# Performance work log

Hardware: AMD Instinct MI355X
Metric: run time of the kernel (lower is better)

The kernel has to match this reference:

```python
import jax, jax.numpy as jnp
import numpy as np

N = 20000      # atoms
E = 320000     # directed edges
F = 128        # feat_dim
NRBF = 20
CUTOFF = 5.0
L = 3          # num_conv
EPS = 1e-15


def swish(x):
    return x * jax.nn.sigmoid(x)


def rbf(dist):
    # PainnRadialBasis: sin(n*pi*d/cutoff)/d, n = 1..NRBF
    n = jnp.arange(1, NRBF + 1, dtype=dist.dtype)
    d = dist[:, None]
    return jnp.sin(n * (jnp.pi / CUTOFF) * d) / d


def cos_envelope(dist):
    return jnp.where(dist < CUTOFF, 0.5 * (jnp.cos(jnp.pi * dist / CUTOFF) + 1.0), 0.0)


def vnorm(v):
    # NFF norm: sqrt(sum(v**2 + EPS))
    return jnp.sqrt(jnp.sum(v * v + EPS, axis=-1))


def setup_inputs() -> dict:
    key = jax.random.key(0)
    ks = jax.random.split(key, 32)
    s = 0.05
    inp = {
        'xyz': jax.random.uniform(ks[0], (N, 3), dtype=jnp.float32),
        'z': jax.random.randint(ks[1], (N,), 0, 100),
        'nbrs': jax.random.randint(ks[2], (E, 2), 0, N),
        # embedding + top-level DistEmb (n_rbf -> F)
        'embed_table': jax.random.normal(ks[3], (100, F), jnp.float32) * s,
        'de_w': jax.random.normal(ks[4], (NRBF, F), jnp.float32) * s,
        'de_b': jax.random.normal(ks[5], (F,), jnp.float32) * s,
        # message blocks (stacked over L layers)
        'msg_w1': jax.random.normal(ks[6], (L, F, F), jnp.float32) * s,
        'msg_b1': jax.random.normal(ks[7], (L, F), jnp.float32) * s,
        'msg_w2': jax.random.normal(ks[8], (L, F, 3 * F), jnp.float32) * s,
        'msg_b2': jax.random.normal(ks[9], (L, 3 * F), jnp.float32) * s,
        'msg_dw': jax.random.normal(ks[10], (L, NRBF, 3 * F), jnp.float32) * s,
        'msg_db': jax.random.normal(ks[11], (L, 3 * F), jnp.float32) * s,
        # update blocks
        'upd_u': jax.random.normal(ks[12], (L, F, F), jnp.float32) * s,
        'upd_v': jax.random.normal(ks[13], (L, F, F), jnp.float32) * s,
        'upd_w1': jax.random.normal(ks[14], (L, 2 * F, F), jnp.float32) * s,
        'upd_b1': jax.random.normal(ks[15], (L, F), jnp.float32) * s,
        'upd_w2': jax.random.normal(ks[16], (L, F, 3 * F), jnp.float32) * s,
        'upd_b2': jax.random.normal(ks[17], (L, 3 * F), jnp.float32) * s,
        # edge update MLPs
        'edge_w1': jax.random.normal(ks[18], (L, F, 2 * F), jnp.float32) * s,
        'edge_b1': jax.random.normal(ks[19], (L, 2 * F), jnp.float32) * s,
        'edge_w2': jax.random.normal(ks[20], (L, 2 * F, F), jnp.float32) * s,
        'edge_b2': jax.random.normal(ks[21], (L, F), jnp.float32) * s,
        # edge readout
        'ro_w1': jax.random.normal(ks[22], (F, 2 * F), jnp.float32) * s,
        'ro_b1': jax.random.normal(ks[23], (2 * F,), jnp.float32) * s,
        'ro_w2': jax.random.normal(ks[24], (2 * F, 1), jnp.float32) * s,
        'ro_b2': jax.random.normal(ks[25], (1,), jnp.float32) * s,
    }
    return inp


def forcepai_forward(xyz, embed_table, de_w, de_b, msg_w1, msg_b1, msg_w2, msg_b2,
                     msg_dw, msg_db, upd_u, upd_v, upd_w1, upd_b1, upd_w2, upd_b2,
                     edge_w1, edge_b1, edge_w2, edge_b2, ro_w1, ro_b1, ro_w2, ro_b2,
                     z, nbrs):
    seg = lambda x, idx: jax.ops.segment_sum(x, idx, num_segments=N)
    src, dst = nbrs[:, 0], nbrs[:, 1]

    r_ij = xyz[dst] - xyz[src]                       # (E, 3)
    dist = vnorm(r_ij)                               # (E,)
    unit = r_ij / dist[:, None]                      # (E, 3) == xyz_adjoint

    rbf_feats = rbf(dist)                            # (E, NRBF)
    env = cos_envelope(dist)[:, None]                # (E, 1)

    s_i = embed_table[z]                             # (N, F)
    v_i = jnp.zeros((N, F, 3), dtype=s_i.dtype)      # (N, F, 3)
    e_ij = (rbf_feats @ de_w + de_b) * env           # (E, F)

    for l in range(L):
        # --- MessageBlock ---
        phi = swish(s_i @ msg_w1[l] + msg_b1[l]) @ msg_w2[l] + msg_b2[l]   # (N, 3F)
        w_s = (rbf_feats @ msg_dw[l] + msg_db[l]) * env                    # (E, 3F)
        inv = (phi[dst] * w_s).reshape(E, 3, F)                            # (E, 3, F)
        split0 = inv[:, 0, :][..., None]                                   # (E, F, 1)
        split1 = inv[:, 1, :]                                              # (E, F)
        split2 = inv[:, 2, :][..., None]                                   # (E, F, 1)
        dv_ij = split2 * unit[:, None, :] + split0 * v_i[dst]              # (E, F, 3)
        s_i = s_i + seg(split1, src)
        v_i = v_i + seg(dv_ij, src)

        # --- UpdateBlock ---
        u_v = jnp.einsum('nfd,fg->ngd', v_i, upd_u[l])                     # (N, F, 3)
        v_v = jnp.einsum('nfd,fg->ngd', v_i, upd_v[l])                     # (N, F, 3)
        stack = jnp.concatenate([s_i, vnorm(v_v)], axis=-1)                # (N, 2F)
        split = (swish(stack @ upd_w1[l] + upd_b1[l]) @ upd_w2[l] + upd_b2[l]).reshape(N, 3, F)
        a_vv = split[:, 0, :][..., None]
        a_sv = split[:, 1, :]
        a_ss = split[:, 2, :]
        v_i = v_i + u_v * a_vv
        s_i = s_i + jnp.sum(u_v * v_v, axis=-1) * a_sv + a_ss

        # --- edge update ---
        pair = s_i[src] + s_i[dst]                                         # (E, F)
        e_ij = e_ij + (swish(pair @ edge_w1[l] + edge_b1[l]) @ edge_w2[l] + edge_b2[l])

    f_edge = (swish(e_ij @ ro_w1 + ro_b1) @ ro_w2 + ro_b2) * unit          # (E, 3)
    f_atom = seg(f_edge, src) - seg(f_edge, dst)                           # (N, 3)
    return f_atom


def reference(xyz, z, nbrs, embed_table, de_w, de_b, msg_w1, msg_b1, msg_w2, msg_b2,
              msg_dw, msg_db, upd_u, upd_v, upd_w1, upd_b1, upd_w2, upd_b2,
              edge_w1, edge_b1, edge_w2, edge_b2, ro_w1, ro_b1, ro_w2, ro_b2):
    return forcepai_forward(xyz, embed_table, de_w, de_b, msg_w1, msg_b1, msg_w2, msg_b2,
                            msg_dw, msg_db, upd_u, upd_v, upd_w1, upd_b1, upd_w2, upd_b2,
                            edge_w1, edge_b1, edge_w2, edge_b2, ro_w1, ro_b1, ro_w2, ro_b2,
                            z, nbrs)
```

## Files before the change

kernel.cpp:

```cpp
#include <hip/hip_runtime.h>

#define NA 20000
#define NE 320000
#define FD 128
#define NRBF 20
#define NL 3
#define PI_F 3.14159265358979323846f

typedef __attribute__((ext_vector_type(8))) short bf16x8;
typedef __attribute__((ext_vector_type(4))) float f32x4;

__device__ float g_unitv[NE*3];
__device__ float g_env[NE];
__device__ float g_rbf[NE*NRBF];
__device__ float g_eij[NE*FD];
__device__ float g_s[NA*FD];
__device__ float g_vA[NA*3*FD];
__device__ float g_vB[NA*3*FD];
__device__ float g_phi[NA*3*FD];
__device__ float g_vv[NA*3*FD];
__device__ float g_stk[NA*2*FD];
__device__ float g_hsm[NA*FD];
__device__ int   g_off[NA+1];
__device__ int   g_cur[NA];
__device__ int   g_eid[NE];
__device__ unsigned short g_w1p[NL*FD*2*FD];
__device__ unsigned short g_w2p[NL*2*FD*FD];
__device__ unsigned short g_rw1p[FD*2*FD];

__device__ __forceinline__ float swishf(float x) { return x / (1.0f + __expf(-x)); }
__device__ __forceinline__ unsigned short f2bf(float x) {
    unsigned int u = __float_as_uint(x);
    unsigned int r = (u + 0x7FFFu + ((u >> 16) & 1u)) >> 16;
    return (unsigned short)r;
}
__device__ __forceinline__ float bf2f(unsigned short u) {
    return __uint_as_float(((unsigned int)u) << 16);
}

__global__ __launch_bounds__(256) void k_geom(const float* __restrict__ xyz, const int* __restrict__ nbrs)
{
    int e = blockIdx.x * 256 + threadIdx.x;
    if (e >= NE) return;
    int si = nbrs[2*e], di = nbrs[2*e+1];
    float rx = xyz[3*di+0] - xyz[3*si+0];
    float ry = xyz[3*di+1] - xyz[3*si+1];
    float rz = xyz[3*di+2] - xyz[3*si+2];
    float d2 = rx*rx + ry*ry + rz*rz + 3e-15f;
    float dist = sqrtf(d2);
    float inv = 1.0f / dist;
    g_unitv[3*e+0] = rx*inv;
    g_unitv[3*e+1] = ry*inv;
    g_unitv[3*e+2] = rz*inv;
    g_env[e] = (dist < 5.0f) ? 0.5f*(cosf(PI_F*dist*0.2f) + 1.0f) : 0.0f;
    #pragma unroll
    for (int k = 0; k < NRBF; ++k)
        g_rbf[(size_t)e*NRBF + k] = sinf((float)(k+1) * (PI_F*0.2f) * dist) * inv;
}

__global__ __launch_bounds__(256) void k_einit(const float* __restrict__ de_w, const float* __restrict__ de_b)
{
    int idx = blockIdx.x * 256 + threadIdx.x;
    if (idx >= NE * FD) return;
    int e = idx >> 7, f = idx & 127;
    float rb[NRBF];
    const float4* rp = reinterpret_cast<const float4*>(g_rbf + (size_t)e*NRBF);
    #pragma unroll
    for (int q = 0; q < 5; ++q) { float4 t = rp[q]; rb[4*q]=t.x; rb[4*q+1]=t.y; rb[4*q+2]=t.z; rb[4*q+3]=t.w; }
    float acc = de_b[f];
    #pragma unroll
    for (int k = 0; k < NRBF; ++k) acc = fmaf(rb[k], de_w[k*FD + f], acc);
    g_eij[(size_t)idx] = acc * g_env[e];
}

__global__ __launch_bounds__(256) void k_embed(const int* __restrict__ z, const float* __restrict__ table)
{
    int idx = blockIdx.x * 256 + threadIdx.x;
    if (idx >= NA * FD) return;
    int n = idx >> 7, f = idx & 127;
    g_s[idx] = table[z[n]*FD + f];
}

__global__ __launch_bounds__(256) void k_zero(float* __restrict__ fout)
{
    int idx = blockIdx.x * 256 + threadIdx.x;
    if (idx < NA*3*FD) g_vA[idx] = 0.f;
    if (idx < NA)      g_cur[idx] = 0;
    if (idx < NA*3)    fout[idx] = 0.f;
}

__global__ __launch_bounds__(256) void k_pack(const float* __restrict__ W, unsigned short* __restrict__ out,
                                              int K, int N)
{
    int idx = blockIdx.x * 256 + threadIdx.x;
    int total = (K >> 5) * (N >> 4) * 64;
    if (idx >= total) return;
    int lane = idx & 63;
    int kc = (idx >> 6) % (K >> 5);
    int nt = (idx >> 6) / (K >> 5);
    int col = nt*16 + (lane & 15);
    int kb  = kc*32 + (lane >> 4) * 8;
    bf16x8 v;
    #pragma unroll
    for (int j = 0; j < 8; ++j) v[j] = (short)f2bf(W[(size_t)(kb + j) * N + col]);
    *reinterpret_cast<bf16x8*>(out + (size_t)idx * 8) = v;
}

__global__ __launch_bounds__(256) void k_count(const int* __restrict__ nbrs)
{
    int e = blockIdx.x * 256 + threadIdx.x;
    if (e < NE) atomicAdd(&g_cur[nbrs[2*e]], 1);
}

__global__ __launch_bounds__(1024) void k_scan()
{
    __shared__ int sd[1024];
    __shared__ int sbase;
    int tid = threadIdx.x;
    if (tid == 0) sbase = 0;
    __syncthreads();
    for (int c0 = 0; c0 < NA; c0 += 1024) {
        int i = c0 + tid;
        int x = (i < NA) ? g_cur[i] : 0;
        sd[tid] = x;
        __syncthreads();
        for (int o = 1; o < 1024; o <<= 1) {
            int t = (tid >= o) ? sd[tid - o] : 0;
            __syncthreads();
            sd[tid] += t;
            __syncthreads();
        }
        if (i < NA) { int excl = sbase + sd[tid] - x; g_off[i] = excl; g_cur[i] = excl; }
        __syncthreads();
        if (tid == 0) sbase += sd[1023];
        __syncthreads();
    }
    if (tid == 0) g_off[NA] = sbase;
}

__global__ __launch_bounds__(256) void k_fill(const int* __restrict__ nbrs)
{
    int e = blockIdx.x * 256 + threadIdx.x;
    if (e < NE) { int p = atomicAdd(&g_cur[nbrs[2*e]], 1); g_eid[p] = e; }
}

#define BM 128
#define BN 128
#define BK 32
#define LDA_S 132
#define LDW_S 132
template<bool SWISH>
__global__ __launch_bounds__(256) void k_gemm(const float* __restrict__ A, const float* __restrict__ W,
        const float* __restrict__ bias, float* __restrict__ C, int R, int K, int Cc)
{
    __shared__ float As[BK * LDA_S];
    __shared__ float Ws[BK * LDW_S];
    int tid = threadIdx.x;
    int row0 = blockIdx.x * BM;
    int col0 = blockIdx.y * BN;
    int tx = tid & 15, ty = tid >> 4;
    float acc[8][8];
    #pragma unroll
    for (int i = 0; i < 8; ++i)
        #pragma unroll
        for (int j = 0; j < 8; ++j) acc[i][j] = 0.f;
    for (int k0 = 0; k0 < K; k0 += BK) {
        #pragma unroll
        for (int i = 0; i < 4; ++i) {
            int fi = tid + i*256;
            int r = fi >> 3, q = fi & 7;
            float4 v = make_float4(0.f, 0.f, 0.f, 0.f);
            int gr = row0 + r;
            if (gr < R) v = *reinterpret_cast<const float4*>(A + (size_t)gr*K + k0 + q*4);
            As[(q*4+0)*LDA_S + r] = v.x;
            As[(q*4+1)*LDA_S + r] = v.y;
            As[(q*4+2)*LDA_S + r] = v.z;
            As[(q*4+3)*LDA_S + r] = v.w;
        }
        #pragma unroll
        for (int i = 0; i < 4; ++i) {
            int fi = tid + i*256;
            int kr = fi >> 5, qq = fi & 31;
            float4 v = *reinterpret_cast<const float4*>(W + (size_t)(k0+kr)*Cc + col0 + qq*4);
            *reinterpret_cast<float4*>(&Ws[kr*LDW_S + qq*4]) = v;
        }
        __syncthreads();
        #pragma unroll
        for (int k = 0; k < BK; ++k) {
            float a[8], w[8];
            *reinterpret_cast<float4*>(&a[0]) = *reinterpret_cast<const float4*>(&As[k*LDA_S + ty*8]);
            *reinterpret_cast<float4*>(&a[4]) = *reinterpret_cast<const float4*>(&As[k*LDA_S + ty*8 + 4]);
            *reinterpret_cast<float4*>(&w[0]) = *reinterpret_cast<const float4*>(&Ws[k*LDW_S + tx*8]);
            *reinterpret_cast<float4*>(&w[4]) = *reinterpret_cast<const float4*>(&Ws[k*LDW_S + tx*8 + 4]);
            #pragma unroll
            for (int i = 0; i < 8; ++i)
                #pragma unroll
                for (int j = 0; j < 8; ++j)
                    acc[i][j] = fmaf(a[i], w[j], acc[i][j]);
        }
        __syncthreads();
    }
    #pragma unroll
    for (int i = 0; i < 8; ++i) {
        int gr = row0 + ty*8 + i;
        if (gr >= R) continue;
        #pragma unroll
        for (int j = 0; j < 8; j += 4) {
            int gc = col0 + tx*8 + j;
            float t[4];
            #pragma unroll
            for (int jj = 0; jj < 4; ++jj) {
                float x = acc[i][j+jj] + (bias ? bias[gc+jj] : 0.f);
                t[jj] = SWISH ? swishf(x) : x;
            }
            float4 o; o.x=t[0]; o.y=t[1]; o.z=t[2]; o.w=t[3];
            *reinterpret_cast<float4*>(C + (size_t)gr*Cc + gc) = o;
        }
    }
}

__global__ __launch_bounds__(128) void k_msg(
        const int* __restrict__ nbrs,
        const float* __restrict__ dw, const float* __restrict__ db,
        const float* __restrict__ vold, float* __restrict__ vnew)
{
    int n = blockIdx.x;
    int f = threadIdx.x;
    float sacc = 0.f, va0 = 0.f, va1 = 0.f, va2 = 0.f;
    int b = g_off[n], eend = g_off[n+1];
    float db0 = db[f], db1 = db[FD + f], db2 = db[2*FD + f];
    for (int ii = b; ii < eend; ++ii) {
        int e = g_eid[ii];
        int dst = nbrs[2*e+1];
        float ev = g_env[e];
        float rb[NRBF];
        const float4* rp = reinterpret_cast<const float4*>(g_rbf + (size_t)e*NRBF);
        #pragma unroll
        for (int q = 0; q < 5; ++q) { float4 t = rp[q]; rb[4*q]=t.x; rb[4*q+1]=t.y; rb[4*q+2]=t.z; rb[4*q+3]=t.w; }
        float w0 = db0, w1 = db1, w2 = db2;
        #pragma unroll
        for (int k = 0; k < NRBF; ++k) {
            float r = rb[k];
            w0 = fmaf(r, dw[k*3*FD + f],        w0);
            w1 = fmaf(r, dw[k*3*FD + FD + f],   w1);
            w2 = fmaf(r, dw[k*3*FD + 2*FD + f], w2);
        }
        w0 *= ev; w1 *= ev; w2 *= ev;
        const float* pd = g_phi + (size_t)dst*3*FD;
        float p0 = pd[f]        * w0;
        float p1 = pd[FD + f]   * w1;
        float p2 = pd[2*FD + f] * w2;
        sacc += p1;
        float ux = g_unitv[3*e+0], uy = g_unitv[3*e+1], uz = g_unitv[3*e+2];
        const float* vd = vold + (size_t)dst*3*FD;
        va0 = fmaf(p2, ux, fmaf(p0, vd[f],        va0));
        va1 = fmaf(p2, uy, fmaf(p0, vd[FD + f],   va1));
        va2 = fmaf(p2, uz, fmaf(p0, vd[2*FD + f], va2));
    }
    size_t nb = (size_t)n*3*FD;
    vnew[nb + f]        = vold[nb + f]        + va0;
    vnew[nb + FD + f]   = vold[nb + FD + f]   + va1;
    vnew[nb + 2*FD + f] = vold[nb + 2*FD + f] + va2;
    g_s[n*FD + f] += sacc;
}

__global__ __launch_bounds__(256) void k_stack()
{
    int idx = blockIdx.x * 256 + threadIdx.x;
    if (idx >= NA * FD) return;
    int n = idx >> 7, f = idx & 127;
    const float* v = g_vv + (size_t)n*3*FD;
    float a = v[f], b = v[FD + f], c = v[2*FD + f];
    float vn = sqrtf(a*a + b*b + c*c + 3e-15f);
    g_stk[(size_t)n*2*FD + f]      = g_s[idx];
    g_stk[(size_t)n*2*FD + FD + f] = vn;
}

__global__ __launch_bounds__(256) void k_apply(const float* __restrict__ split, float* __restrict__ v)
{
    int idx = blockIdx.x * 256 + threadIdx.x;
    if (idx >= NA * FD) return;
    int n = idx >> 7, f = idx & 127;
    const float* sp = split + (size_t)n*3*FD;
    float avv = sp[f], asv = sp[FD + f], ass = sp[2*FD + f];
    size_t nb = (size_t)n*3*FD;
    float dot = 0.f;
    #pragma unroll
    for (int d = 0; d < 3; ++d) {
        float u = g_phi[nb + d*FD + f], w = g_vv[nb + d*FD + f];
        v[nb + d*FD + f] += u * avv;
        dot = fmaf(u, w, dot);
    }
    g_s[idx] += dot * asv + ass;
}

__global__ __launch_bounds__(256) void k_edge_mfma(
        const int* __restrict__ nbrs,
        const unsigned short* __restrict__ w1p, const float* __restrict__ b1,
        const unsigned short* __restrict__ w2p, const float* __restrict__ b2)
{
    __shared__ unsigned short pairA[64*128];
    __shared__ unsigned short hid[64*256];
    int tid = threadIdx.x;
    int e0 = blockIdx.x * 64;

    #pragma unroll
    for (int i = 0; i < 4; ++i) {
        int idx = i*256 + tid;
        int r = idx >> 4, c8 = idx & 15;
        int e = e0 + r;
        int si = nbrs[2*e], di = nbrs[2*e+1];
        const float4* ps = reinterpret_cast<const float4*>(g_s + (size_t)si*FD + c8*8);
        const float4* pq = reinterpret_cast<const float4*>(g_s + (size_t)di*FD + c8*8);
        float4 a0 = ps[0], a1 = ps[1], d0 = pq[0], d1 = pq[1];
        bf16x8 v;
        v[0]=(short)f2bf(a0.x+d0.x); v[1]=(short)f2bf(a0.y+d0.y);
        v[2]=(short)f2bf(a0.z+d0.z); v[3]=(short)f2bf(a0.w+d0.w);
        v[4]=(short)f2bf(a1.x+d1.x); v[5]=(short)f2bf(a1.y+d1.y);
        v[6]=(short)f2bf(a1.z+d1.z); v[7]=(short)f2bf(a1.w+d1.w);
        int byte = (r*256 + c8*16) ^ ((r & 7) << 4);
        *reinterpret_cast<bf16x8*>(reinterpret_cast<char*>(pairA) + byte) = v;
    }
    __syncthreads();

    int lane = tid & 63, w = tid >> 6;
    int r0 = w * 16;
    int arow = r0 + (lane & 15);
    int crow = r0 + ((lane >> 4) << 2);
    int ccol = lane & 15;

    bf16x8 a1f[4];
    #pragma unroll
    for (int kc = 0; kc < 4; ++kc) {
        int byte = (arow*256 + kc*64 + (lane >> 4)*16) ^ ((arow & 7) << 4);
        a1f[kc] = *reinterpret_cast<const bf16x8*>(reinterpret_cast<const char*>(pairA) + byte);
    }
    #pragma unroll 4
    for (int nt = 0; nt < 16; ++nt) {
        f32x4 acc = {0.f, 0.f, 0.f, 0.f};
        #pragma unroll
        for (int kc = 0; kc < 4; ++kc) {
            bf16x8 bv = *reinterpret_cast<const bf16x8*>(w1p + ((size_t)(nt*4 + kc)*64 + lane)*8);
            acc = __builtin_amdgcn_mfma_f32_16x16x32_bf16(a1f[kc], bv, acc, 0, 0, 0);
        }
        int col = nt*16 + ccol;
        float bb = b1[col];
        #pragma unroll
        for (int i = 0; i < 4; ++i) {
            int row = crow + i;
            float h = swishf(acc[i] + bb);
            int byte = (row*512 + col*2) ^ ((row & 7) << 4);
            *reinterpret_cast<unsigned short*>(reinterpret_cast<char*>(hid) + byte) = f2bf(h);
        }
    }
    bf16x8 a2f[8];
    #pragma unroll
    for (int kc = 0; kc < 8; ++kc) {
        int byte = (arow*512 + kc*64 + (lane >> 4)*16) ^ ((arow & 7) << 4);
        a2f[kc] = *reinterpret_cast<const bf16x8*>(reinterpret_cast<const char*>(hid) + byte);
    }
    #pragma unroll 4
    for (int nt = 0; nt < 8; ++nt) {
        f32x4 acc = {0.f, 0.f, 0.f, 0.f};
        #pragma unroll
        for (int kc = 0; kc < 8; ++kc) {
            bf16x8 bv = *reinterpret_cast<const bf16x8*>(w2p + ((size_t)(nt*8 + kc)*64 + lane)*8);
            acc = __builtin_amdgcn_mfma_f32_16x16x32_bf16(a2f[kc], bv, acc, 0, 0, 0);
        }
        int col = nt*16 + ccol;
        float bb = b2[col];
        #pragma unroll
        for (int i = 0; i < 4; ++i) {
            int row = crow + i;
            float* p = g_eij + (size_t)(e0 + row)*FD + col;
            *p += acc[i] + bb;
        }
    }
}

__global__ __launch_bounds__(256) void k_readout_mfma(
        const int* __restrict__ nbrs,
        const unsigned short* __restrict__ w1p, const float* __restrict__ b1,
        const float* __restrict__ w2, const float* __restrict__ b2,
        float* __restrict__ fatom)
{
    __shared__ unsigned short pairA[64*128];
    __shared__ unsigned short hid[64*256];
    int tid = threadIdx.x;
    int e0 = blockIdx.x * 64;

    #pragma unroll
    for (int i = 0; i < 4; ++i) {
        int idx = i*256 + tid;
        int r = idx >> 4, c8 = idx & 15;
        const float4* ps = reinterpret_cast<const float4*>(g_eij + (size_t)(e0 + r)*FD + c8*8);
        float4 a0 = ps[0], a1 = ps[1];
        bf16x8 v;
        v[0]=(short)f2bf(a0.x); v[1]=(short)f2bf(a0.y); v[2]=(short)f2bf(a0.z); v[3]=(short)f2bf(a0.w);
        v[4]=(short)f2bf(a1.x); v[5]=(short)f2bf(a1.y); v[6]=(short)f2bf(a1.z); v[7]=(short)f2bf(a1.w);
        int byte = (r*256 + c8*16) ^ ((r & 7) << 4);
        *reinterpret_cast<bf16x8*>(reinterpret_cast<char*>(pairA) + byte) = v;
    }
    __syncthreads();

    int lane = tid & 63, w = tid >> 6;
    int r0 = w * 16;
    int arow = r0 + (lane & 15);
    int crow = r0 + ((lane >> 4) << 2);
    int ccol = lane & 15;

    bf16x8 a1f[4];
    #pragma unroll
    for (int kc = 0; kc < 4; ++kc) {
        int byte = (arow*256 + kc*64 + (lane >> 4)*16) ^ ((arow & 7) << 4);
        a1f[kc] = *reinterpret_cast<const bf16x8*>(reinterpret_cast<const char*>(pairA) + byte);
    }
    #pragma unroll 4
    for (int nt = 0; nt < 16; ++nt) {
        f32x4 acc = {0.f, 0.f, 0.f, 0.f};
        #pragma unroll
        for (int kc = 0; kc < 4; ++kc) {
            bf16x8 bv = *reinterpret_cast<const bf16x8*>(w1p + ((size_t)(nt*4 + kc)*64 + lane)*8);
            acc = __builtin_amdgcn_mfma_f32_16x16x32_bf16(a1f[kc], bv, acc, 0, 0, 0);
        }
        int col = nt*16 + ccol;
        float bb = b1[col];
        #pragma unroll
        for (int i = 0; i < 4; ++i) {
            int row = crow + i;
            float h = swishf(acc[i] + bb);
            int byte = (row*512 + col*2) ^ ((row & 7) << 4);
            *reinterpret_cast<unsigned short*>(reinterpret_cast<char*>(hid) + byte) = f2bf(h);
        }
    }
    int erow = r0 + (lane >> 2);
    int kp = lane & 3;
    float part = 0.f;
    #pragma unroll
    for (int cc = 0; cc < 8; ++cc) {
        int byte = (erow*512 + kp*128 + cc*16) ^ ((erow & 7) << 4);
        bf16x8 hv = *reinterpret_cast<const bf16x8*>(reinterpret_cast<const char*>(hid) + byte);
        const float* wp = w2 + kp*64 + cc*8;
        #pragma unroll
        for (int j = 0; j < 8; ++j)
            part = fmaf(bf2f((unsigned short)hv[j]), wp[j], part);
    }
    part += __shfl_xor(part, 1);
    part += __shfl_xor(part, 2);
    if (kp == 0) {
        int e = e0 + erow;
        float sc = part + b2[0];
        int si = nbrs[2*e], di = nbrs[2*e+1];
        #pragma unroll
        for (int d = 0; d < 3; ++d) {
            float fe = sc * g_unitv[3*e+d];
            atomicAdd(&fatom[3*si+d], fe);
            atomicAdd(&fatom[3*di+d], -fe);
        }
    }
}

extern "C" void kernel_launch(void* const* d_in, const int* in_sizes, int n_in,
                              void* d_out, int out_size, void* d_ws, size_t ws_size,
                              hipStream_t stream)
{
    (void)in_sizes; (void)n_in; (void)out_size; (void)d_ws; (void)ws_size;
    const float* xyz    = (const float*)d_in[0];
    const int*   z      = (const int*)  d_in[1];
    const int*   nbrs   = (const int*)  d_in[2];
    const float* emb    = (const float*)d_in[3];
    const float* de_w   = (const float*)d_in[4];
    const float* de_b   = (const float*)d_in[5];
    const float* msg_w1 = (const float*)d_in[6];
    const float* msg_b1 = (const float*)d_in[7];
    const float* msg_w2 = (const float*)d_in[8];
    const float* msg_b2 = (const float*)d_in[9];
    const float* msg_dw = (const float*)d_in[10];
    const float* msg_db = (const float*)d_in[11];
    const float* upd_u  = (const float*)d_in[12];
    const float* upd_v  = (const float*)d_in[13];
    const float* upd_w1 = (const float*)d_in[14];
    const float* upd_b1 = (const float*)d_in[15];
    const float* upd_w2 = (const float*)d_in[16];
    const float* upd_b2 = (const float*)d_in[17];
    const float* edge_w1= (const float*)d_in[18];
    const float* edge_b1= (const float*)d_in[19];
    const float* edge_w2= (const float*)d_in[20];
    const float* edge_b2= (const float*)d_in[21];
    const float* ro_w1  = (const float*)d_in[22];
    const float* ro_b1  = (const float*)d_in[23];
    const float* ro_w2  = (const float*)d_in[24];
    const float* ro_b2  = (const float*)d_in[25];
    float* fout = (float*)d_out;

    void *p_vA = nullptr, *p_vB = nullptr, *p_phi = nullptr, *p_vv = nullptr,
         *p_stk = nullptr, *p_hsm = nullptr, *p_s = nullptr,
         *p_w1p = nullptr, *p_w2p = nullptr, *p_rw1p = nullptr;
    hipGetSymbolAddress(&p_vA,   HIP_SYMBOL(g_vA));
    hipGetSymbolAddress(&p_vB,   HIP_SYMBOL(g_vB));
    hipGetSymbolAddress(&p_phi,  HIP_SYMBOL(g_phi));
    hipGetSymbolAddress(&p_vv,   HIP_SYMBOL(g_vv));
    hipGetSymbolAddress(&p_stk,  HIP_SYMBOL(g_stk));
    hipGetSymbolAddress(&p_hsm,  HIP_SYMBOL(g_hsm));
    hipGetSymbolAddress(&p_s,    HIP_SYMBOL(g_s));
    hipGetSymbolAddress(&p_w1p,  HIP_SYMBOL(g_w1p));
    hipGetSymbolAddress(&p_w2p,  HIP_SYMBOL(g_w2p));
    hipGetSymbolAddress(&p_rw1p, HIP_SYMBOL(g_rw1p));
    float* vA  = (float*)p_vA;
    float* vB  = (float*)p_vB;
    float* phi = (float*)p_phi;
    float* vv  = (float*)p_vv;
    float* stk = (float*)p_stk;
    float* hsm = (float*)p_hsm;
    float* sft = (float*)p_s;
    unsigned short* w1p  = (unsigned short*)p_w1p;
    unsigned short* w2p  = (unsigned short*)p_w2p;
    unsigned short* rw1p = (unsigned short*)p_rw1p;

    k_zero <<<(NA*3*FD+255)/256, 256, 0, stream>>>(fout);
    k_geom <<<(NE+255)/256, 256, 0, stream>>>(xyz, nbrs);
    k_einit<<<(NE*FD+255)/256, 256, 0, stream>>>(de_w, de_b);
    k_embed<<<(NA*FD+255)/256, 256, 0, stream>>>(z, emb);
    k_count<<<(NE+255)/256, 256, 0, stream>>>(nbrs);
    k_scan <<<1, 1024, 0, stream>>>();
    k_fill <<<(NE+255)/256, 256, 0, stream>>>(nbrs);
    for (int l = 0; l < NL; ++l) {
        k_pack<<<16, 256, 0, stream>>>(edge_w1 + (size_t)l*FD*2*FD, w1p + (size_t)l*FD*2*FD, FD, 2*FD);
        k_pack<<<16, 256, 0, stream>>>(edge_w2 + (size_t)l*2*FD*FD, w2p + (size_t)l*2*FD*FD, 2*FD, FD);
    }
    k_pack<<<16, 256, 0, stream>>>(ro_w1, rw1p, FD, 2*FD);

    const int gN  = (NA + BM - 1) / BM;
    const int g3N = (3*NA + BM - 1) / BM;
    for (int l = 0; l < NL; ++l) {
        float* vOld = (l & 1) ? vB : vA;
        float* vNew = (l & 1) ? vA : vB;
        const float* mw1 = msg_w1 + (size_t)l*FD*FD;
        const float* mb1 = msg_b1 + (size_t)l*FD;
        const float* mw2 = msg_w2 + (size_t)l*FD*3*FD;
        const float* mb2 = msg_b2 + (size_t)l*3*FD;
        const float* mdw = msg_dw + (size_t)l*NRBF*3*FD;
        const float* mdb = msg_db + (size_t)l*3*FD;
        const float* uu  = upd_u  + (size_t)l*FD*FD;
        const float* uvw = upd_v  + (size_t)l*FD*FD;
        const float* uw1 = upd_w1 + (size_t)l*2*FD*FD;
        const float* ub1 = upd_b1 + (size_t)l*FD;
        const float* uw2 = upd_w2 + (size_t)l*FD*3*FD;
        const float* ub2 = upd_b2 + (size_t)l*3*FD;
        const float* eb1 = edge_b1 + (size_t)l*2*FD;
        const float* eb2 = edge_b2 + (size_t)l*FD;

        k_gemm<true> <<<dim3(gN,1), 256, 0, stream>>>(sft, mw1, mb1, hsm, NA, FD, FD);
        k_gemm<false><<<dim3(gN,3), 256, 0, stream>>>(hsm, mw2, mb2, phi, NA, FD, 3*FD);
        k_msg<<<NA, FD, 0, stream>>>(nbrs, mdw, mdb, vOld, vNew);
        k_gemm<false><<<dim3(g3N,1), 256, 0, stream>>>(vNew, uu,  nullptr, phi, 3*NA, FD, FD);
        k_gemm<false><<<dim3(g3N,1), 256, 0, stream>>>(vNew, uvw, nullptr, vv,  3*NA, FD, FD);
        k_stack<<<(NA*FD+255)/256, 256, 0, stream>>>();
        k_gemm<true> <<<dim3(gN,1), 256, 0, stream>>>(stk, uw1, ub1, hsm, NA, 2*FD, FD);
        k_gemm<false><<<dim3(gN,3), 256, 0, stream>>>(hsm, uw2, ub2, vOld , NA, FD, 3*FD);
        k_apply<<<(NA*FD+255)/256, 256, 0, stream>>>(vOld, vNew);
        k_edge_mfma<<<NE/64, 256, 0, stream>>>(nbrs, w1p + (size_t)l*FD*2*FD, eb1,
                                               w2p + (size_t)l*2*FD*FD, eb2);
    }
    k_readout_mfma<<<NE/64, 256, 0, stream>>>(nbrs, rw1p, ro_b1, ro_w2, ro_b2, fout);
}
```

Baseline: 2.998 ms.

## Fuse edge init, all edge-update layers and readout into one register-resident kernel

Edge features e_ij stop living in global memory. Each layer takes a bf16 snapshot of the atom scalars, and one fused kernel per 64-edge block computes the RBF embedding, runs all three edge MLP updates with e_ij held in MFMA accumulators, then does the readout. This removes the 160MB fp32 e_ij buffer's repeated read-modify-write traffic plus the k_einit and per-layer edge/readout launches. It works only because edge states never feed back into the atom updates. The cost is more register pressure from holding 8 accumulator tiles, and a bf16 rounding of s before the pair sum.

```diff
diff --git a/kernel.cpp b/kernel.cpp
--- a/kernel.cpp
+++ b/kernel.cpp
@@ -13,7 +13,6 @@
 __device__ float g_unitv[NE*3];
 __device__ float g_env[NE];
 __device__ float g_rbf[NE*NRBF];
-__device__ float g_eij[NE*FD];
 __device__ float g_s[NA*FD];
 __device__ float g_vA[NA*3*FD];
 __device__ float g_vB[NA*3*FD];
@@ -24,6 +23,7 @@
 __device__ int   g_off[NA+1];
 __device__ int   g_cur[NA];
 __device__ int   g_eid[NE];
+__device__ unsigned short g_sb[NL*NA*FD];
 __device__ unsigned short g_w1p[NL*FD*2*FD];
 __device__ unsigned short g_w2p[NL*2*FD*FD];
 __device__ unsigned short g_rw1p[FD*2*FD];
@@ -58,21 +58,6 @@
         g_rbf[(size_t)e*NRBF + k] = sinf((float)(k+1) * (PI_F*0.2f) * dist) * inv;
 }
 
-__global__ __launch_bounds__(256) void k_einit(const float* __restrict__ de_w, const float* __restrict__ de_b)
-{
-    int idx = blockIdx.x * 256 + threadIdx.x;
-    if (idx >= NE * FD) return;
-    int e = idx >> 7, f = idx & 127;
-    float rb[NRBF];
-    const float4* rp = reinterpret_cast<const float4*>(g_rbf + (size_t)e*NRBF);
-    #pragma unroll
-    for (int q = 0; q < 5; ++q) { float4 t = rp[q]; rb[4*q]=t.x; rb[4*q+1]=t.y; rb[4*q+2]=t.z; rb[4*q+3]=t.w; }
-    float acc = de_b[f];
-    #pragma unroll
-    for (int k = 0; k < NRBF; ++k) acc = fmaf(rb[k], de_w[k*FD + f], acc);
-    g_eij[(size_t)idx] = acc * g_env[e];
-}
-
 __global__ __launch_bounds__(256) void k_embed(const int* __restrict__ z, const float* __restrict__ table)
 {
     int idx = blockIdx.x * 256 + threadIdx.x;
@@ -87,6 +72,12 @@
     if (idx < NA*3*FD) g_vA[idx] = 0.f;
     if (idx < NA)      g_cur[idx] = 0;
     if (idx < NA*3)    fout[idx] = 0.f;
+}
+
+__global__ __launch_bounds__(256) void k_snap(int l)
+{
+    int idx = blockIdx.x * 256 + threadIdx.x;
+    if (idx < NA*FD) g_sb[(size_t)l*NA*FD + idx] = f2bf(g_s[idx]);
 }
 
 __global__ __launch_bounds__(256) void k_pack(const float* __restrict__ W, unsigned short* __restrict__ out,
@@ -294,32 +285,34 @@
     g_s[idx] += dot * asv + ass;
 }
 
-__global__ __launch_bounds__(256) void k_edge_mfma(
+__global__ __launch_bounds__(256) void k_edge_fused(
         const int* __restrict__ nbrs,
-        const unsigned short* __restrict__ w1p, const float* __restrict__ b1,
-        const unsigned short* __restrict__ w2p, const float* __restrict__ b2)
+        const float* __restrict__ de_w, const float* __restrict__ de_b,
+        const float* __restrict__ eb1, const float* __restrict__ eb2,
+        const float* __restrict__ ro_b1, const float* __restrict__ ro_w2,
+        const float* __restrict__ ro_b2, float* __restrict__ fatom)
 {
     __shared__ unsigned short pairA[64*128];
     __shared__ unsigned short hid[64*256];
+    __shared__ int nbrL[128];
     int tid = threadIdx.x;
     int e0 = blockIdx.x * 64;
 
-    #pragma unroll
-    for (int i = 0; i < 4; ++i) {
-        int idx = i*256 + tid;
-        int r = idx >> 4, c8 = idx & 15;
-        int e = e0 + r;
-        int si = nbrs[2*e], di = nbrs[2*e+1];
-        const float4* ps = reinterpret_cast<const float4*>(g_s + (size_t)si*FD + c8*8);
-        const float4* pq = reinterpret_cast<const float4*>(g_s + (size_t)di*FD + c8*8);
-        float4 a0 = ps[0], a1 = ps[1], d0 = pq[0], d1 = pq[1];
-        bf16x8 v;
-        v[0]=(short)f2bf(a0.x+d0.x); v[1]=(short)f2bf(a0.y+d0.y);
-        v[2]=(short)f2bf(a0.z+d0.z); v[3]=(short)f2bf(a0.w+d0.w);
-        v[4]=(short)f2bf(a1.x+d1.x); v[5]=(short)f2bf(a1.y+d1.y);
-        v[6]=(short)f2bf(a1.z+d1.z); v[7]=(short)f2bf(a1.w+d1.w);
-        int byte = (r*256 + c8*16) ^ ((r & 7) << 4);
-        *reinterpret_cast<bf16x8*>(reinterpret_cast<char*>(pairA) + byte) = v;
+    float* rbfL  = reinterpret_cast<float*>(pairA);
+    float* envL  = rbfL + 64*NRBF;
+    float* de_wL = reinterpret_cast<float*>(hid);
+
+    if (tid < 128) nbrL[tid] = nbrs[2*e0 + tid];
+    #pragma unroll
+    for (int i = 0; i < 5; ++i) {
+        int j = i*256 + tid;
+        if (j < 64*NRBF) rbfL[j] = g_rbf[(size_t)e0*NRBF + j];
+    }
+    if (tid < 64) envL[tid] = g_env[e0 + tid];
+    #pragma unroll
+    for (int i = 0; i < 10; ++i) {
+        int j = i*256 + tid;
+        de_wL[j] = de_w[j];
     }
     __syncthreads();
 
@@ -329,6 +322,107 @@
     int crow = r0 + ((lane >> 4) << 2);
     int ccol = lane & 15;
 
+    f32x4 acc_e[8];
+    #pragma unroll
+    for (int nt = 0; nt < 8; ++nt) acc_e[nt] = f32x4{0.f, 0.f, 0.f, 0.f};
+    #pragma unroll 4
+    for (int k = 0; k < NRBF; ++k) {
+        float rb[4];
+        #pragma unroll
+        for (int i = 0; i < 4; ++i) rb[i] = rbfL[(crow + i)*NRBF + k];
+        #pragma unroll
+        for (int nt = 0; nt < 8; ++nt) {
+            float wv = de_wL[k*FD + nt*16 + ccol];
+            #pragma unroll
+            for (int i = 0; i < 4; ++i) acc_e[nt][i] = fmaf(rb[i], wv, acc_e[nt][i]);
+        }
+    }
+    #pragma unroll
+    for (int nt = 0; nt < 8; ++nt) {
+        float bb = de_b[nt*16 + ccol];
+        #pragma unroll
+        for (int i = 0; i < 4; ++i) acc_e[nt][i] = (acc_e[nt][i] + bb) * envL[crow + i];
+    }
+
+    for (int l = 0; l < NL; ++l) {
+        __syncthreads();
+        const unsigned short* sb = g_sb + (size_t)l*NA*FD;
+        #pragma unroll
+        for (int i = 0; i < 4; ++i) {
+            int idx = i*256 + tid;
+            int r = idx >> 4, c8 = idx & 15;
+            int si = nbrL[2*r], di = nbrL[2*r+1];
+            bf16x8 a = *reinterpret_cast<const bf16x8*>(sb + (size_t)si*FD + c8*8);
+            bf16x8 b = *reinterpret_cast<const bf16x8*>(sb + (size_t)di*FD + c8*8);
+            bf16x8 v;
+            #pragma unroll
+            for (int j = 0; j < 8; ++j)
+                v[j] = (short)f2bf(bf2f((unsigned short)a[j]) + bf2f((unsigned short)b[j]));
+            int byte = (r*256 + c8*16) ^ ((r & 7) << 4);
+            *reinterpret_cast<bf16x8*>(reinterpret_cast<char*>(pairA) + byte) = v;
+        }
+        __syncthreads();
+
+        const unsigned short* w1l = g_w1p + (size_t)l*FD*2*FD;
+        const unsigned short* w2l = g_w2p + (size_t)l*2*FD*FD;
+        const float* b1l = eb1 + (size_t)l*2*FD;
+        const float* b2l = eb2 + (size_t)l*FD;
+
+        bf16x8 a1f[4];
+        #pragma unroll
+        for (int kc = 0; kc < 4; ++kc) {
+            int byte = (arow*256 + kc*64 + (lane >> 4)*16) ^ ((arow & 7) << 4);
+            a1f[kc] = *reinterpret_cast<const bf16x8*>(reinterpret_cast<const char*>(pairA) + byte);
+        }
+        #pragma unroll 4
+        for (int nt = 0; nt < 16; ++nt) {
+            f32x4 acc = f32x4{0.f, 0.f, 0.f, 0.f};
+            #pragma unroll
+            for (int kc = 0; kc < 4; ++kc) {
+                bf16x8 bv = *reinterpret_cast<const bf16x8*>(w1l + ((size_t)(nt*4 + kc)*64 + lane)*8);
+                acc = __builtin_amdgcn_mfma_f32_16x16x32_bf16(a1f[kc], bv, acc, 0, 0, 0);
+            }
+            int col = nt*16 + ccol;
+            float bb = b1l[col];
+            #pragma unroll
+            for (int i = 0; i < 4; ++i) {
+                int row = crow + i;
+                float h = swishf(acc[i] + bb);
+                int byte = (row*512 + col*2) ^ ((row & 7) << 4);
+                *reinterpret_cast<unsigned short*>(reinterpret_cast<char*>(hid) + byte) = f2bf(h);
+            }
+        }
+        bf16x8 a2f[8];
+        #pragma unroll
+        for (int kc = 0; kc < 8; ++kc) {
+            int byte = (arow*512 + kc*64 + (lane >> 4)*16) ^ ((arow & 7) << 4);
+            a2f[kc] = *reinterpret_cast<const bf16x8*>(reinterpret_cast<const char*>(hid) + byte);
+        }
+        #pragma unroll 4
+        for (int nt = 0; nt < 8; ++nt) {
+            f32x4 acc = acc_e[nt];
+            #pragma unroll
+            for (int kc = 0; kc < 8; ++kc) {
+                bf16x8 bv = *reinterpret_cast<const bf16x8*>(w2l + ((size_t)(nt*8 + kc)*64 + lane)*8);
+                acc = __builtin_amdgcn_mfma_f32_16x16x32_bf16(a2f[kc], bv, acc, 0, 0, 0);
+            }
+            float bb = b2l[nt*16 + ccol];
+            #pragma unroll
+            for (int i = 0; i < 4; ++i) acc[i] += bb;
+            acc_e[nt] = acc;
+        }
+    }
+
+    #pragma unroll
+    for (int nt = 0; nt < 8; ++nt) {
+        int col = nt*16 + ccol;
+        #pragma unroll
+        for (int i = 0; i < 4; ++i) {
+            int row = crow + i;
+            int byte = (row*256 + col*2) ^ ((row & 7) << 4);
+            *reinterpret_cast<unsigned short*>(reinterpret_cast<char*>(pairA) + byte) = f2bf(acc_e[nt][i]);
+        }
+    }
     bf16x8 a1f[4];
     #pragma unroll
     for (int kc = 0; kc < 4; ++kc) {
@@ -337,14 +431,14 @@
     }
     #pragma unroll 4
     for (int nt = 0; nt < 16; ++nt) {
-        f32x4 acc = {0.f, 0.f, 0.f, 0.f};
+        f32x4 acc = f32x4{0.f, 0.f, 0.f, 0.f};
         #pragma unroll
         for (int kc = 0; kc < 4; ++kc) {
-            bf16x8 bv = *reinterpret_cast<const bf16x8*>(w1p + ((size_t)(nt*4 + kc)*64 + lane)*8);
+            bf16x8 bv = *reinterpret_cast<const bf16x8*>(g_rw1p + ((size_t)(nt*4 + kc)*64 + lane)*8);
             acc = __builtin_amdgcn_mfma_f32_16x16x32_bf16(a1f[kc], bv, acc, 0, 0, 0);
         }
         int col = nt*16 + ccol;
-        float bb = b1[col];
+        float bb = ro_b1[col];
         #pragma unroll
         for (int i = 0; i < 4; ++i) {
             int row = crow + i;
@@ -353,86 +447,6 @@
             *reinterpret_cast<unsigned short*>(reinterpret_cast<char*>(hid) + byte) = f2bf(h);
         }
     }
-    bf16x8 a2f[8];
-    #pragma unroll
-    for (int kc = 0; kc < 8; ++kc) {
-        int byte = (arow*512 + kc*64 + (lane >> 4)*16) ^ ((arow & 7) << 4);
-        a2f[kc] = *reinterpret_cast<const bf16x8*>(reinterpret_cast<const char*>(hid) + byte);
-    }
-    #pragma unroll 4
-    for (int nt = 0; nt < 8; ++nt) {
-        f32x4 acc = {0.f, 0.f, 0.f, 0.f};
-        #pragma unroll
-        for (int kc = 0; kc < 8; ++kc) {
-            bf16x8 bv = *reinterpret_cast<const bf16x8*>(w2p + ((size_t)(nt*8 + kc)*64 + lane)*8);
-            acc = __builtin_amdgcn_mfma_f32_16x16x32_bf16(a2f[kc], bv, acc, 0, 0, 0);
-        }
-        int col = nt*16 + ccol;
-        float bb = b2[col];
-        #pragma unroll
-        for (int i = 0; i < 4; ++i) {
-            int row = crow + i;
-            float* p = g_eij + (size_t)(e0 + row)*FD + col;
-            *p += acc[i] + bb;
-        }
-    }
-}
-
-__global__ __launch_bounds__(256) void k_readout_mfma(
-        const int* __restrict__ nbrs,
-        const unsigned short* __restrict__ w1p, const float* __restrict__ b1,
-        const float* __restrict__ w2, const float* __restrict__ b2,
-        float* __restrict__ fatom)
-{
-    __shared__ unsigned short pairA[64*128];
-    __shared__ unsigned short hid[64*256];
-    int tid = threadIdx.x;
-    int e0 = blockIdx.x * 64;
-
-    #pragma unroll
-    for (int i = 0; i < 4; ++i) {
-        int idx = i*256 + tid;
-        int r = idx >> 4, c8 = idx & 15;
-        const float4* ps = reinterpret_cast<const float4*>(g_eij + (size_t)(e0 + r)*FD + c8*8);
-        float4 a0 = ps[0], a1 = ps[1];
-        bf16x8 v;
-        v[0]=(short)f2bf(a0.x); v[1]=(short)f2bf(a0.y); v[2]=(short)f2bf(a0.z); v[3]=(short)f2bf(a0.w);
-        v[4]=(short)f2bf(a1.x); v[5]=(short)f2bf(a1.y); v[6]=(short)f2bf(a1.z); v[7]=(short)f2bf(a1.w);
-        int byte = (r*256 + c8*16) ^ ((r & 7) << 4);
-        *reinterpret_cast<bf16x8*>(reinterpret_cast<char*>(pairA) + byte) = v;
-    }
-    __syncthreads();
-
-    int lane = tid & 63, w = tid >> 6;
-    int r0 = w * 16;
-    int arow = r0 + (lane & 15);
-    int crow = r0 + ((lane >> 4) << 2);
-    int ccol = lane & 15;
-
-    bf16x8 a1f[4];
-    #pragma unroll
-    for (int kc = 0; kc < 4; ++kc) {
-        int byte = (arow*256 + kc*64 + (lane >> 4)*16) ^ ((arow & 7) << 4);
-        a1f[kc] = *reinterpret_cast<const bf16x8*>(reinterpret_cast<const char*>(pairA) + byte);
-    }
-    #pragma unroll 4
-    for (int nt = 0; nt < 16; ++nt) {
-        f32x4 acc = {0.f, 0.f, 0.f, 0.f};
-        #pragma unroll
-        for (int kc = 0; kc < 4; ++kc) {
-            bf16x8 bv = *reinterpret_cast<const bf16x8*>(w1p + ((size_t)(nt*4 + kc)*64 + lane)*8);
-            acc = __builtin_amdgcn_mfma_f32_16x16x32_bf16(a1f[kc], bv, acc, 0, 0, 0);
-        }
-        int col = nt*16 + ccol;
-        float bb = b1[col];
-        #pragma unroll
-        for (int i = 0; i < 4; ++i) {
-            int row = crow + i;
-            float h = swishf(acc[i] + bb);
-            int byte = (row*512 + col*2) ^ ((row & 7) << 4);
-            *reinterpret_cast<unsigned short*>(reinterpret_cast<char*>(hid) + byte) = f2bf(h);
-        }
-    }
     int erow = r0 + (lane >> 2);
     int kp = lane & 3;
     float part = 0.f;
@@ -440,7 +454,7 @@
     for (int cc = 0; cc < 8; ++cc) {
         int byte = (erow*512 + kp*128 + cc*16) ^ ((erow & 7) << 4);
         bf16x8 hv = *reinterpret_cast<const bf16x8*>(reinterpret_cast<const char*>(hid) + byte);
-        const float* wp = w2 + kp*64 + cc*8;
+        const float* wp = ro_w2 + kp*64 + cc*8;
         #pragma unroll
         for (int j = 0; j < 8; ++j)
             part = fmaf(bf2f((unsigned short)hv[j]), wp[j], part);
@@ -449,8 +463,8 @@
     part += __shfl_xor(part, 2);
     if (kp == 0) {
         int e = e0 + erow;
-        float sc = part + b2[0];
-        int si = nbrs[2*e], di = nbrs[2*e+1];
+        float sc = part + ro_b2[0];
+        int si = nbrL[2*erow], di = nbrL[2*erow+1];
         #pragma unroll
         for (int d = 0; d < 3; ++d) {
             float fe = sc * g_unitv[3*e+d];
@@ -519,7 +533,6 @@
 
     k_zero <<<(NA*3*FD+255)/256, 256, 0, stream>>>(fout);
     k_geom <<<(NE+255)/256, 256, 0, stream>>>(xyz, nbrs);
-    k_einit<<<(NE*FD+255)/256, 256, 0, stream>>>(de_w, de_b);
     k_embed<<<(NA*FD+255)/256, 256, 0, stream>>>(z, emb);
     k_count<<<(NE+255)/256, 256, 0, stream>>>(nbrs);
     k_scan <<<1, 1024, 0, stream>>>();
@@ -547,8 +560,6 @@
         const float* ub1 = upd_b1 + (size_t)l*FD;
         const float* uw2 = upd_w2 + (size_t)l*FD*3*FD;
         const float* ub2 = upd_b2 + (size_t)l*3*FD;
-        const float* eb1 = edge_b1 + (size_t)l*2*FD;
-        const float* eb2 = edge_b2 + (size_t)l*FD;
 
         k_gemm<true> <<<dim3(gN,1), 256, 0, stream>>>(sft, mw1, mb1, hsm, NA, FD, FD);
         k_gemm<false><<<dim3(gN,3), 256, 0, stream>>>(hsm, mw2, mb2, phi, NA, FD, 3*FD);
@@ -559,8 +570,8 @@
         k_gemm<true> <<<dim3(gN,1), 256, 0, stream>>>(stk, uw1, ub1, hsm, NA, 2*FD, FD);
         k_gemm<false><<<dim3(gN,3), 256, 0, stream>>>(hsm, uw2, ub2, vOld , NA, FD, 3*FD);
         k_apply<<<(NA*FD+255)/256, 256, 0, stream>>>(vOld, vNew);
-        k_edge_mfma<<<NE/64, 256, 0, stream>>>(nbrs, w1p + (size_t)l*FD*2*FD, eb1,
-                                               w2p + (size_t)l*2*FD*FD, eb2);
-    }
-    k_readout_mfma<<<NE/64, 256, 0, stream>>>(nbrs, rw1p, ro_b1, ro_w2, ro_b2, fout);
-}
+        k_snap<<<(NA*FD+255)/256, 256, 0, stream>>>(l);
+    }
+    k_edge_fused<<<NE/64, 256, 0, stream>>>(nbrs, de_w, de_b, edge_b1, edge_b2,
+                                            ro_b1, ro_w2, ro_b2, fout);
+}
```

After: 2.545 ms. 1.18x faster.
